# Kernel optimization log

Hardware: AMD Instinct MI355X
Metric: run time of the kernel (lower is better)

## Reference

```python
import jax, jax.numpy as jnp
import numpy as np


def setup_inputs() -> dict:
    key = jax.random.key(0)
    k1, k2, k3, k4 = jax.random.split(key, 4)
    B, S, IN, OUT = 4, 2048, 4096, 4096
    x = jax.random.normal(k1, (B, S, IN), dtype=jnp.float32)
    # 4-bit signed range [-8, 7], stored widened (torch uses int8)
    weight_quantized = jax.random.randint(k2, (OUT, IN), -8, 8, dtype=jnp.int32)
    # per-output-row scale, positive and small (abs-max / 7 style)
    weight_scale = jax.random.uniform(k3, (OUT,), dtype=jnp.float32) * 0.01 + 1e-4
    bias = jax.random.normal(k4, (OUT,), dtype=jnp.float32) * 0.01
    return {"x": x, "weight_quantized": weight_quantized,
            "weight_scale": weight_scale, "bias": bias}


def reference(x, weight_quantized, weight_scale, bias):
    # dequantize: [OUT, IN] int -> fp32 scaled per output row
    w = weight_quantized.astype(jnp.float32) * weight_scale[:, None]
    # F.linear: x @ w.T + bias  -> [B, S, OUT]
    out = jnp.einsum('bsi,oi->bso', x, w) + bias
    return out
```

## Files before the change

### kernel.cpp

```cpp
#include <hip/hip_runtime.h>
#include <hip/hip_bf16.h>

typedef __bf16 bf16x4 __attribute__((ext_vector_type(4)));
typedef __bf16 bf16x8 __attribute__((ext_vector_type(8)));
typedef float  floatx4 __attribute__((ext_vector_type(4)));

#define AS1 __attribute__((address_space(1)))
#define AS3 __attribute__((address_space(3)))

__global__ __launch_bounds__(256)
void cvt_both8(const float* __restrict__ xin, const int* __restrict__ win,
               __bf16* __restrict__ xout, __bf16* __restrict__ wout,
               int nx8, int nw8)
{
    const int stride = gridDim.x * 256;
    const int total  = nx8 + nw8;
    for (int i = blockIdx.x * 256 + threadIdx.x; i < total; i += stride) {
        if (i < nx8) {
            const float4* p = reinterpret_cast<const float4*>(xin) + (size_t)i * 2;
            float4 a = p[0], b = p[1];
            bf16x8 h;
            h[0] = (__bf16)a.x; h[1] = (__bf16)a.y; h[2] = (__bf16)a.z; h[3] = (__bf16)a.w;
            h[4] = (__bf16)b.x; h[5] = (__bf16)b.y; h[6] = (__bf16)b.z; h[7] = (__bf16)b.w;
            reinterpret_cast<bf16x8*>(xout)[i] = h;
        } else {
            int j = i - nx8;
            const int4* p = reinterpret_cast<const int4*>(win) + (size_t)j * 2;
            int4 a = p[0], b = p[1];
            bf16x8 h;
            h[0] = (__bf16)(float)a.x; h[1] = (__bf16)(float)a.y;
            h[2] = (__bf16)(float)a.z; h[3] = (__bf16)(float)a.w;
            h[4] = (__bf16)(float)b.x; h[5] = (__bf16)(float)b.y;
            h[6] = (__bf16)(float)b.z; h[7] = (__bf16)(float)b.w;
            reinterpret_cast<bf16x8*>(wout)[j] = h;
        }
    }
}

#define BM2 256
#define BN2 256
#define BK2 64

#define BARRIER() asm volatile("s_barrier" ::: "memory")

template<int P>
__device__ __forceinline__ void mfma_cluster(floatx4 (&acc)[8][4],
                                             const bf16x8 (&af)[2][2],
                                             const bf16x8 (&bfr)[4][2])
{
    __builtin_amdgcn_s_setprio(1);
#pragma unroll
    for (int h = 0; h < 2; ++h)
#pragma unroll
        for (int ii = 0; ii < 2; ++ii)
#pragma unroll
            for (int j = 0; j < 4; ++j)
                acc[2 * P + ii][j] = __builtin_amdgcn_mfma_f32_16x16x32_bf16(
                    af[ii][h], bfr[j][h], acc[2 * P + ii][j], 0, 0, 0);
    __builtin_amdgcn_s_setprio(0);
}

__device__ __forceinline__ void read_af(bf16x8 (&dst)[2][2], const __bf16* cA,
                                        int rowBase, int lm, int kq, int sw)
{
#pragma unroll
    for (int ii = 0; ii < 2; ++ii)
#pragma unroll
        for (int h = 0; h < 2; ++h)
            dst[ii][h] = *reinterpret_cast<const bf16x8*>(
                &cA[(rowBase + ii * 16 + lm) * BK2 + ((kq + h * 4) ^ sw) * 8]);
}

__device__ __forceinline__ void read_bf(bf16x8 (&dst)[4][2], const __bf16* cB,
                                        int wn, int lm, int kq, int sw)
{
#pragma unroll
    for (int j = 0; j < 4; ++j)
#pragma unroll
        for (int h = 0; h < 2; ++h)
            dst[j][h] = *reinterpret_cast<const bf16x8*>(
                &cB[(wn + j * 16 + lm) * BK2 + ((kq + h * 4) ^ sw) * 8]);
}

__global__ __launch_bounds__(512)
void gemm_bf16_bt_pipe(const __bf16* __restrict__ A, const __bf16* __restrict__ B,
                       const float* __restrict__ scale, const float* __restrict__ bias,
                       float* __restrict__ Out, int M, int N, int K)
{
    __shared__ __bf16 sA[2][BM2 * BK2];
    __shared__ __bf16 sB[2][BN2 * BK2];

    const int tid  = threadIdx.x;
    const int wave = tid >> 6;
    const int lane = tid & 63;
    const int row0 = blockIdx.y * BM2;
    const int col0 = blockIdx.x * BN2;

    const int sRow = lane >> 3;
    const int gBlk = (lane & 7) ^ sRow;
    const size_t aBase = (size_t)(row0 + wave * 8 + sRow) * K + gBlk * 8;
    const size_t bBase = (size_t)(col0 + wave * 8 + sRow) * K + gBlk * 8;
    const int ldsWOff = wave * 8 * BK2;

#define STAGE_A(buf, q, kt_) \
    __builtin_amdgcn_global_load_lds( \
        (const AS1 void*)(A + aBase + (size_t)(q) * 64 * K + (size_t)(kt_) * BK2), \
        (AS3 void*)&sA[(buf)][(q) * 64 * BK2 + ldsWOff], 16, 0, 0)
#define STAGE_B(buf, q, kt_) \
    __builtin_amdgcn_global_load_lds( \
        (const AS1 void*)(B + bBase + (size_t)(q) * 64 * K + (size_t)(kt_) * BK2), \
        (AS3 void*)&sB[(buf)][(q) * 64 * BK2 + ldsWOff], 16, 0, 0)

    const int wm = (wave >> 2) * 128;
    const int wn = (wave & 3) * 64;
    const int lm = lane & 15;
    const int kq = lane >> 4;
    const int sw = lm & 7;

    floatx4 acc[8][4];
#pragma unroll
    for (int i = 0; i < 8; ++i)
#pragma unroll
        for (int j = 0; j < 4; ++j)
            acc[i][j] = (floatx4)0.0f;

    bf16x8 bfr[4][2];
    bf16x8 afE[2][2];
    bf16x8 afO[2][2];
    const int nt = K / BK2;

    STAGE_A(0, 0, 0); STAGE_A(0, 2, 0);
    STAGE_B(0, 0, 0); STAGE_B(0, 1, 0); STAGE_B(0, 2, 0); STAGE_B(0, 3, 0);
    STAGE_A(0, 1, 0); STAGE_A(0, 3, 0);
    STAGE_B(1, 0, 1); STAGE_B(1, 1, 1); STAGE_B(1, 2, 1); STAGE_B(1, 3, 1);
    STAGE_A(1, 0, 1); STAGE_A(1, 2, 1);
    asm volatile("s_waitcnt vmcnt(8)" ::: "memory");
    BARRIER();
    read_bf(bfr, sB[0], wn, lm, kq, sw);
    read_af(afE, sA[0], wm, lm, kq, sw);

#define TILE(c, n1, n2)                                                        \
                                                                       \
    STAGE_A((c) ^ 1, 1, n1); STAGE_A((c) ^ 1, 3, n1);                          \
    mfma_cluster<0>(acc, afE, bfr);                                            \
    read_af(afO, sA[(c)], wm + 32, lm, kq, sw);                                \
    asm volatile("s_waitcnt vmcnt(8)" ::: "memory");                           \
    BARRIER();                                                                 \
                                                                       \
    STAGE_B((c), 0, n2); STAGE_B((c), 1, n2);                                  \
    STAGE_B((c), 2, n2); STAGE_B((c), 3, n2);                                  \
    mfma_cluster<1>(acc, afO, bfr);                                            \
    read_af(afE, sA[(c)], wm + 64, lm, kq, sw);                                \
    BARRIER();                                                                 \
                                                                       \
    STAGE_A((c), 0, n2); STAGE_A((c), 2, n2);                                  \
    mfma_cluster<2>(acc, afE, bfr);                                            \
    read_af(afO, sA[(c)], wm + 96, lm, kq, sw);                                \
    asm volatile("s_waitcnt vmcnt(8)" ::: "memory");                           \
    BARRIER();                                                                 \
                                                                       \
    mfma_cluster<3>(acc, afO, bfr);                                            \
    read_bf(bfr, sB[(c) ^ 1], wn, lm, kq, sw);                                 \
    read_af(afE, sA[(c) ^ 1], wm, lm, kq, sw);                                 \
    BARRIER();

    for (int it = 0; it < nt / 2; ++it) {
        const int kt = 2 * it;
        const int e1 = kt + 1;
        const int e2 = (kt + 2 < nt) ? kt + 2 : 0;
        const int o2 = (kt + 3 < nt) ? kt + 3 : 0;
        TILE(0, e1, e2)
        TILE(1, e2, o2)
    }
    asm volatile("s_waitcnt vmcnt(0)" ::: "memory");
#undef TILE
#undef STAGE_A
#undef STAGE_B

#pragma unroll
    for (int j = 0; j < 4; ++j) {
        int n = col0 + wn + j * 16 + lm;
        float sc = scale[n];
        float bi = bias[n];
#pragma unroll
        for (int i = 0; i < 8; ++i) {
#pragma unroll
            for (int r = 0; r < 4; ++r) {
                int m = row0 + wm + i * 16 + kq * 4 + r;
                Out[(size_t)m * N + n] = sc * acc[i][j][r] + bi;
            }
        }
    }
}

#define BM 128
#define BN 128
#define BK 64

__global__ __launch_bounds__(256)
void gemm_bf16_bt(const __bf16* __restrict__ A, const __bf16* __restrict__ B,
                  const float* __restrict__ scale, const float* __restrict__ bias,
                  float* __restrict__ Out, int M, int N, int K)
{
    __shared__ __bf16 sA[BM * BK];
    __shared__ __bf16 sB[BN * BK];

    const int tid  = threadIdx.x;
    const int row0 = blockIdx.y * BM;
    const int col0 = blockIdx.x * BN;
    const int wave = tid >> 6;
    const int lane = tid & 63;

    const int sRow = lane >> 3;
    const int gBlk = (lane & 7) ^ sRow;
    size_t aOff[4], bOff[4];
    const __bf16* ldsA[4];
    const __bf16* ldsB[4];
#pragma unroll
    for (int q = 0; q < 4; ++q) {
        int r = wave * 32 + q * 8 + sRow;
        aOff[q] = (size_t)(row0 + r) * K + gBlk * 8;
        bOff[q] = (size_t)(col0 + r) * K + gBlk * 8;
        ldsA[q] = &sA[(wave * 32 + q * 8) * BK];
        ldsB[q] = &sB[(wave * 32 + q * 8) * BK];
    }

    const int wm = (wave >> 1) * 64;
    const int wn = (wave & 1) * 64;
    const int lm = lane & 15;
    const int kq = lane >> 4;
    const int sw = lm & 7;

    floatx4 acc[4][4];
#pragma unroll
    for (int i = 0; i < 4; ++i)
#pragma unroll
        for (int j = 0; j < 4; ++j)
            acc[i][j] = (floatx4)0.0f;

    for (int k0 = 0; k0 < K; k0 += BK) {
#pragma unroll
        for (int q = 0; q < 4; ++q) {
            __builtin_amdgcn_global_load_lds((const AS1 void*)(A + aOff[q] + k0),
                                             (AS3 void*)ldsA[q], 16, 0, 0);
            __builtin_amdgcn_global_load_lds((const AS1 void*)(B + bOff[q] + k0),
                                             (AS3 void*)ldsB[q], 16, 0, 0);
        }
        __syncthreads();

#pragma unroll
        for (int h = 0; h < 2; ++h) {
            const int blkA = (kq + h * 4);
            bf16x8 af[4], bfr[4];
#pragma unroll
            for (int i = 0; i < 4; ++i) {
                int row = wm + i * 16 + lm;
                af[i] = *reinterpret_cast<const bf16x8*>(
                            &sA[row * BK + (blkA ^ sw) * 8]);
            }
#pragma unroll
            for (int j = 0; j < 4; ++j) {
                int row = wn + j * 16 + lm;
                bfr[j] = *reinterpret_cast<const bf16x8*>(
                            &sB[row * BK + (blkA ^ sw) * 8]);
            }
#pragma unroll
            for (int i = 0; i < 4; ++i)
#pragma unroll
                for (int j = 0; j < 4; ++j)
                    acc[i][j] = __builtin_amdgcn_mfma_f32_16x16x32_bf16(
                                    af[i], bfr[j], acc[i][j], 0, 0, 0);
        }
        __syncthreads();
    }

#pragma unroll
    for (int j = 0; j < 4; ++j) {
        int n = col0 + wn + j * 16 + lm;
        float sc = scale[n];
        float bi = bias[n];
#pragma unroll
        for (int i = 0; i < 4; ++i) {
#pragma unroll
            for (int r = 0; r < 4; ++r) {
                int m = row0 + wm + i * 16 + kq * 4 + r;
                Out[(size_t)m * N + n] = sc * acc[i][j][r] + bi;
            }
        }
    }
}

__global__ __launch_bounds__(256)
void fp4linear_gemm(const float* __restrict__ X, const int* __restrict__ W,
                    const float* __restrict__ scale, const float* __restrict__ bias,
                    float* __restrict__ Out, int M, int N, int K)
{
    __shared__ __bf16 sA[BM * 32];
    __shared__ __bf16 sB[BN * 32];

    const int tid  = threadIdx.x;
    const int row0 = blockIdx.y * BM;
    const int col0 = blockIdx.x * BN;
    const int wave = tid >> 6;
    const int lane = tid & 63;
    const int wm = (wave >> 1) * 64;
    const int wn = (wave & 1) * 64;
    const int lm = lane & 15;
    const int kq = lane >> 4;

    floatx4 acc[4][4];
#pragma unroll
    for (int i = 0; i < 4; ++i)
#pragma unroll
        for (int j = 0; j < 4; ++j)
            acc[i][j] = (floatx4)0.0f;

    for (int k0 = 0; k0 < K; k0 += 32) {
        float4 fa[4];
        int4   ib[4];
#pragma unroll
        for (int l = 0; l < 4; ++l) {
            int idx = tid + l * 256;
            int r = idx >> 3, c4 = idx & 7;
            fa[l] = *reinterpret_cast<const float4*>(
                        &X[(size_t)(row0 + r) * K + k0 + c4 * 4]);
        }
#pragma unroll
        for (int l = 0; l < 4; ++l) {
            int idx = tid + l * 256;
            int r = idx >> 3, c4 = idx & 7;
            ib[l] = *reinterpret_cast<const int4*>(
                        &W[(size_t)(col0 + r) * K + k0 + c4 * 4]);
        }
        __syncthreads();
#pragma unroll
        for (int l = 0; l < 4; ++l) {
            int idx = tid + l * 256;
            int r = idx >> 3, c4 = idx & 7;
            bf16x4 h;
            h[0] = (__bf16)fa[l].x; h[1] = (__bf16)fa[l].y;
            h[2] = (__bf16)fa[l].z; h[3] = (__bf16)fa[l].w;
            *reinterpret_cast<bf16x4*>(&sA[r * 32 + c4 * 4]) = h;
        }
#pragma unroll
        for (int l = 0; l < 4; ++l) {
            int idx = tid + l * 256;
            int r = idx >> 3, c4 = idx & 7;
            bf16x4 h;
            h[0] = (__bf16)(float)ib[l].x; h[1] = (__bf16)(float)ib[l].y;
            h[2] = (__bf16)(float)ib[l].z; h[3] = (__bf16)(float)ib[l].w;
            *reinterpret_cast<bf16x4*>(&sB[r * 32 + c4 * 4]) = h;
        }
        __syncthreads();

        bf16x8 af[4], bfr[4];
#pragma unroll
        for (int i = 0; i < 4; ++i)
            af[i] = *reinterpret_cast<const bf16x8*>(
                        &sA[(wm + i * 16 + lm) * 32 + kq * 8]);
#pragma unroll
        for (int j = 0; j < 4; ++j)
            bfr[j] = *reinterpret_cast<const bf16x8*>(
                        &sB[(wn + j * 16 + lm) * 32 + kq * 8]);
#pragma unroll
        for (int i = 0; i < 4; ++i)
#pragma unroll
            for (int j = 0; j < 4; ++j)
                acc[i][j] = __builtin_amdgcn_mfma_f32_16x16x32_bf16(
                                af[i], bfr[j], acc[i][j], 0, 0, 0);
    }

#pragma unroll
    for (int j = 0; j < 4; ++j) {
        int n = col0 + wn + j * 16 + lm;
        float sc = scale[n];
        float bi = bias[n];
#pragma unroll
        for (int i = 0; i < 4; ++i) {
#pragma unroll
            for (int r = 0; r < 4; ++r) {
                int m = row0 + wm + i * 16 + kq * 4 + r;
                Out[(size_t)m * N + n] = sc * acc[i][j][r] + bi;
            }
        }
    }
}

extern "C" void kernel_launch(void* const* d_in, const int* in_sizes, int n_in,
                              void* d_out, int out_size, void* d_ws, size_t ws_size,
                              hipStream_t stream) {
    const float* x     = (const float*)d_in[0];
    const int*   wq    = (const int*)d_in[1];
    const float* scale = (const float*)d_in[2];
    const float* bias  = (const float*)d_in[3];
    float* out = (float*)d_out;

    const int N = in_sizes[2];
    const int K = in_sizes[1] / N;
    const int M = in_sizes[0] / K;

    const size_t xElems = (size_t)M * K;
    const size_t wElems = (size_t)N * K;
    const size_t need   = (xElems + wElems) * sizeof(__bf16);

    const bool cvt_ok = (ws_size >= need) && (xElems % 8 == 0) && (wElems % 8 == 0);
    const int  nt     = K / BK2;

    if (cvt_ok) {
        __bf16* xb = (__bf16*)d_ws;
        __bf16* wb = xb + xElems;
        int nx8 = (int)(xElems / 8);
        int nw8 = (int)(wElems / 8);
        int total = nx8 + nw8;
        int cvtBlocks = (total + 255) / 256;
        if (cvtBlocks > 2048) cvtBlocks = 2048;
        hipLaunchKernelGGL(cvt_both8, dim3(cvtBlocks), dim3(256), 0, stream,
                           x, wq, xb, wb, nx8, nw8);
        if ((M % BM2 == 0) && (N % BN2 == 0) && (K % BK2 == 0) &&
            (nt % 2 == 0) && (nt >= 4)) {
            hipLaunchKernelGGL(gemm_bf16_bt_pipe, dim3(N / BN2, M / BM2), dim3(512),
                               0, stream, xb, wb, scale, bias, out, M, N, K);
        } else if ((M % BM == 0) && (N % BN == 0) && (K % BK == 0)) {
            hipLaunchKernelGGL(gemm_bf16_bt, dim3(N / BN, M / BM), dim3(256),
                               0, stream, xb, wb, scale, bias, out, M, N, K);
        } else {
            hipLaunchKernelGGL(fp4linear_gemm, dim3(N / BN, M / BM), dim3(256),
                               0, stream, x, wq, scale, bias, out, M, N, K);
        }
    } else {
        hipLaunchKernelGGL(fp4linear_gemm, dim3(N / BN, M / BM), dim3(256), 0, stream,
                           x, wq, scale, bias, out, M, N, K);
    }
}
```

Baseline: 507.0 us.

## Fuse conversion and GEMM into one cooperative persistent kernel with grid sync

Merges the fp32/int to bf16 conversion and the pipelined GEMM into a single cooperative kernel. The grid converts both operands, synchronizes across the whole grid, then loops persistently over 256x256 output tiles. This removes one kernel launch and the gap between kernels. The trade-offs are a grid-wide barrier, a grid capped at 256 blocks (so M=8192, N=4096 gives 512 tiles and two rounds per block), and slightly reordered LDS reads relative to the MFMA clusters. It also drops the 128x128 fallback GEMM path.

```diff
diff --git a/kernel.cpp b/kernel.cpp
--- a/kernel.cpp
+++ b/kernel.cpp
@@ -1,5 +1,8 @@
 #include <hip/hip_runtime.h>
 #include <hip/hip_bf16.h>
+#include <hip/hip_cooperative_groups.h>
+
+namespace cg = cooperative_groups;
 
 typedef __bf16 bf16x4 __attribute__((ext_vector_type(4)));
 typedef __bf16 bf16x8 __attribute__((ext_vector_type(8)));
@@ -7,6 +10,199 @@
 
 #define AS1 __attribute__((address_space(1)))
 #define AS3 __attribute__((address_space(3)))
+
+#define BM2 256
+#define BN2 256
+#define BK2 64
+
+#define BARRIER() asm volatile("s_barrier" ::: "memory")
+
+template<int P>
+__device__ __forceinline__ void mfma_cluster(floatx4 (&acc)[8][4],
+                                             const bf16x8 (&af)[2][2],
+                                             const bf16x8 (&bfr)[4][2])
+{
+    __builtin_amdgcn_s_setprio(1);
+#pragma unroll
+    for (int h = 0; h < 2; ++h)
+#pragma unroll
+        for (int ii = 0; ii < 2; ++ii)
+#pragma unroll
+            for (int j = 0; j < 4; ++j)
+                acc[2 * P + ii][j] = __builtin_amdgcn_mfma_f32_16x16x32_bf16(
+                    af[ii][h], bfr[j][h], acc[2 * P + ii][j], 0, 0, 0);
+    __builtin_amdgcn_s_setprio(0);
+}
+
+__device__ __forceinline__ void read_af(bf16x8 (&dst)[2][2], const __bf16* cA,
+                                        int rowBase, int lm, int kq, int sw)
+{
+#pragma unroll
+    for (int ii = 0; ii < 2; ++ii)
+#pragma unroll
+        for (int h = 0; h < 2; ++h)
+            dst[ii][h] = *reinterpret_cast<const bf16x8*>(
+                &cA[(rowBase + ii * 16 + lm) * BK2 + ((kq + h * 4) ^ sw) * 8]);
+}
+
+__device__ __forceinline__ void read_bf(bf16x8 (&dst)[4][2], const __bf16* cB,
+                                        int wn, int lm, int kq, int sw)
+{
+#pragma unroll
+    for (int j = 0; j < 4; ++j)
+#pragma unroll
+        for (int h = 0; h < 2; ++h)
+            dst[j][h] = *reinterpret_cast<const bf16x8*>(
+                &cB[(wn + j * 16 + lm) * BK2 + ((kq + h * 4) ^ sw) * 8]);
+}
+
+__device__ __forceinline__ void gemm_tile256(
+    __bf16* sAp, __bf16* sBp,
+    const __bf16* __restrict__ A, const __bf16* __restrict__ B,
+    const float* __restrict__ scale, const float* __restrict__ bias,
+    float* __restrict__ Out, int N, int K, int row0, int col0,
+    int wave, int lane)
+{
+    const int sRow = lane >> 3;
+    const int gBlk = (lane & 7) ^ sRow;
+    const size_t aBase = (size_t)(row0 + wave * 8 + sRow) * K + gBlk * 8;
+    const size_t bBase = (size_t)(col0 + wave * 8 + sRow) * K + gBlk * 8;
+    const int ldsWOff = wave * 8 * BK2;
+
+#define STAGE_A(buf, q, kt_) \
+    __builtin_amdgcn_global_load_lds( \
+        (const AS1 void*)(A + aBase + (size_t)(q) * 64 * K + (size_t)(kt_) * BK2), \
+        (AS3 void*)(sAp + (buf) * (BM2 * BK2) + (q) * 64 * BK2 + ldsWOff), 16, 0, 0)
+#define STAGE_B(buf, q, kt_) \
+    __builtin_amdgcn_global_load_lds( \
+        (const AS1 void*)(B + bBase + (size_t)(q) * 64 * K + (size_t)(kt_) * BK2), \
+        (AS3 void*)(sBp + (buf) * (BN2 * BK2) + (q) * 64 * BK2 + ldsWOff), 16, 0, 0)
+
+    const int wm = (wave >> 2) * 128;
+    const int wn = (wave & 3) * 64;
+    const int lm = lane & 15;
+    const int kq = lane >> 4;
+    const int sw = lm & 7;
+
+    floatx4 acc[8][4];
+#pragma unroll
+    for (int i = 0; i < 8; ++i)
+#pragma unroll
+        for (int j = 0; j < 4; ++j)
+            acc[i][j] = (floatx4)0.0f;
+
+    bf16x8 bfr[4][2];
+    bf16x8 afE[2][2];
+    bf16x8 afO[2][2];
+    const int nt = K / BK2;
+
+    STAGE_A(0, 0, 0); STAGE_A(0, 2, 0);
+    STAGE_B(0, 0, 0); STAGE_B(0, 1, 0); STAGE_B(0, 2, 0); STAGE_B(0, 3, 0);
+    STAGE_A(0, 1, 0); STAGE_A(0, 3, 0);
+    STAGE_B(1, 0, 1); STAGE_B(1, 1, 1); STAGE_B(1, 2, 1); STAGE_B(1, 3, 1);
+    STAGE_A(1, 0, 1); STAGE_A(1, 2, 1);
+    asm volatile("s_waitcnt vmcnt(8)" ::: "memory");
+    BARRIER();
+    read_bf(bfr, sBp, wn, lm, kq, sw);
+    read_af(afE, sAp, wm, lm, kq, sw);
+
+#define TILE(c, n1, n2)                                                        \
+                                                                       \
+    STAGE_A((c) ^ 1, 1, n1); STAGE_A((c) ^ 1, 3, n1);                          \
+    read_af(afO, sAp + (c) * (BM2 * BK2), wm + 32, lm, kq, sw);                \
+    mfma_cluster<0>(acc, afE, bfr);                                            \
+    asm volatile("s_waitcnt vmcnt(8)" ::: "memory");                           \
+    BARRIER();                                                                 \
+                                                                       \
+    STAGE_B((c), 0, n2); STAGE_B((c), 1, n2);                                  \
+    STAGE_B((c), 2, n2); STAGE_B((c), 3, n2);                                  \
+    read_af(afE, sAp + (c) * (BM2 * BK2), wm + 64, lm, kq, sw);                \
+    mfma_cluster<1>(acc, afO, bfr);                                            \
+    BARRIER();                                                                 \
+                                                                       \
+    STAGE_A((c), 0, n2); STAGE_A((c), 2, n2);                                  \
+    read_af(afO, sAp + (c) * (BM2 * BK2), wm + 96, lm, kq, sw);                \
+    mfma_cluster<2>(acc, afE, bfr);                                            \
+    asm volatile("s_waitcnt vmcnt(8)" ::: "memory");                           \
+    BARRIER();                                                                 \
+                                                                       \
+    read_af(afE, sAp + ((c) ^ 1) * (BM2 * BK2), wm, lm, kq, sw);               \
+    mfma_cluster<3>(acc, afO, bfr);                                            \
+    read_bf(bfr, sBp + ((c) ^ 1) * (BN2 * BK2), wn, lm, kq, sw);               \
+    BARRIER();
+
+    for (int it = 0; it < nt / 2; ++it) {
+        const int kt = 2 * it;
+        const int e1 = kt + 1;
+        const int e2 = (kt + 2 < nt) ? kt + 2 : 0;
+        const int o2 = (kt + 3 < nt) ? kt + 3 : 0;
+        TILE(0, e1, e2)
+        TILE(1, e2, o2)
+    }
+    asm volatile("s_waitcnt vmcnt(0)" ::: "memory");
+#undef TILE
+#undef STAGE_A
+#undef STAGE_B
+
+#pragma unroll
+    for (int j = 0; j < 4; ++j) {
+        int n = col0 + wn + j * 16 + lm;
+        float sc = scale[n];
+        float bi = bias[n];
+#pragma unroll
+        for (int i = 0; i < 8; ++i) {
+#pragma unroll
+            for (int r = 0; r < 4; ++r) {
+                int m = row0 + wm + i * 16 + kq * 4 + r;
+                Out[(size_t)m * N + n] = sc * acc[i][j][r] + bi;
+            }
+        }
+    }
+}
+
+__global__ __launch_bounds__(512)
+void fused_coop(const float* __restrict__ xin, const int* __restrict__ win,
+                const float* __restrict__ scale, const float* __restrict__ bias,
+                float* __restrict__ out, __bf16* __restrict__ xb,
+                __bf16* __restrict__ wb, int M, int N, int K, int nx8, int nw8)
+{
+    {
+        const int stride = gridDim.x * 512;
+        const int total  = nx8 + nw8;
+        for (int i = blockIdx.x * 512 + threadIdx.x; i < total; i += stride) {
+            if (i < nx8) {
+                const float4* p = reinterpret_cast<const float4*>(xin) + (size_t)i * 2;
+                float4 a = p[0], b = p[1];
+                bf16x8 h;
+                h[0] = (__bf16)a.x; h[1] = (__bf16)a.y; h[2] = (__bf16)a.z; h[3] = (__bf16)a.w;
+                h[4] = (__bf16)b.x; h[5] = (__bf16)b.y; h[6] = (__bf16)b.z; h[7] = (__bf16)b.w;
+                reinterpret_cast<bf16x8*>(xb)[i] = h;
+            } else {
+                int j = i - nx8;
+                const int4* p = reinterpret_cast<const int4*>(win) + (size_t)j * 2;
+                int4 a = p[0], b = p[1];
+                bf16x8 h;
+                h[0] = (__bf16)(float)a.x; h[1] = (__bf16)(float)a.y;
+                h[2] = (__bf16)(float)a.z; h[3] = (__bf16)(float)a.w;
+                h[4] = (__bf16)(float)b.x; h[5] = (__bf16)(float)b.y;
+                h[6] = (__bf16)(float)b.z; h[7] = (__bf16)(float)b.w;
+                reinterpret_cast<bf16x8*>(wb)[j] = h;
+            }
+        }
+    }
+    cg::this_grid().sync();
+
+    __shared__ __bf16 sA[2 * BM2 * BK2];
+    __shared__ __bf16 sB[2 * BN2 * BK2];
+    const int wave = threadIdx.x >> 6;
+    const int lane = threadIdx.x & 63;
+    const int nbx = N / BN2;
+    const int nTiles = (M / BM2) * nbx;
+    for (int t = blockIdx.x; t < nTiles; t += gridDim.x) {
+        gemm_tile256(sA, sB, xb, wb, scale, bias, out, N, K,
+                     (t / nbx) * BM2, (t % nbx) * BN2, wave, lane);
+    }
+}
 
 __global__ __launch_bounds__(256)
 void cvt_both8(const float* __restrict__ xin, const int* __restrict__ win,
@@ -37,258 +233,20 @@
     }
 }
 
-#define BM2 256
-#define BN2 256
-#define BK2 64
-
-#define BARRIER() asm volatile("s_barrier" ::: "memory")
-
-template<int P>
-__device__ __forceinline__ void mfma_cluster(floatx4 (&acc)[8][4],
-                                             const bf16x8 (&af)[2][2],
-                                             const bf16x8 (&bfr)[4][2])
-{
-    __builtin_amdgcn_s_setprio(1);
-#pragma unroll
-    for (int h = 0; h < 2; ++h)
-#pragma unroll
-        for (int ii = 0; ii < 2; ++ii)
-#pragma unroll
-            for (int j = 0; j < 4; ++j)
-                acc[2 * P + ii][j] = __builtin_amdgcn_mfma_f32_16x16x32_bf16(
-                    af[ii][h], bfr[j][h], acc[2 * P + ii][j], 0, 0, 0);
-    __builtin_amdgcn_s_setprio(0);
-}
-
-__device__ __forceinline__ void read_af(bf16x8 (&dst)[2][2], const __bf16* cA,
-                                        int rowBase, int lm, int kq, int sw)
-{
-#pragma unroll
-    for (int ii = 0; ii < 2; ++ii)
-#pragma unroll
-        for (int h = 0; h < 2; ++h)
-            dst[ii][h] = *reinterpret_cast<const bf16x8*>(
-                &cA[(rowBase + ii * 16 + lm) * BK2 + ((kq + h * 4) ^ sw) * 8]);
-}
-
-__device__ __forceinline__ void read_bf(bf16x8 (&dst)[4][2], const __bf16* cB,
-                                        int wn, int lm, int kq, int sw)
-{
-#pragma unroll
-    for (int j = 0; j < 4; ++j)
-#pragma unroll
-        for (int h = 0; h < 2; ++h)
-            dst[j][h] = *reinterpret_cast<const bf16x8*>(
-                &cB[(wn + j * 16 + lm) * BK2 + ((kq + h * 4) ^ sw) * 8]);
-}
-
 __global__ __launch_bounds__(512)
 void gemm_bf16_bt_pipe(const __bf16* __restrict__ A, const __bf16* __restrict__ B,
                        const float* __restrict__ scale, const float* __restrict__ bias,
                        float* __restrict__ Out, int M, int N, int K)
 {
-    __shared__ __bf16 sA[2][BM2 * BK2];
-    __shared__ __bf16 sB[2][BN2 * BK2];
-
-    const int tid  = threadIdx.x;
-    const int wave = tid >> 6;
-    const int lane = tid & 63;
-    const int row0 = blockIdx.y * BM2;
-    const int col0 = blockIdx.x * BN2;
-
-    const int sRow = lane >> 3;
-    const int gBlk = (lane & 7) ^ sRow;
-    const size_t aBase = (size_t)(row0 + wave * 8 + sRow) * K + gBlk * 8;
-    const size_t bBase = (size_t)(col0 + wave * 8 + sRow) * K + gBlk * 8;
-    const int ldsWOff = wave * 8 * BK2;
-
-#define STAGE_A(buf, q, kt_) \
-    __builtin_amdgcn_global_load_lds( \
-        (const AS1 void*)(A + aBase + (size_t)(q) * 64 * K + (size_t)(kt_) * BK2), \
-        (AS3 void*)&sA[(buf)][(q) * 64 * BK2 + ldsWOff], 16, 0, 0)
-#define STAGE_B(buf, q, kt_) \
-    __builtin_amdgcn_global_load_lds( \
-        (const AS1 void*)(B + bBase + (size_t)(q) * 64 * K + (size_t)(kt_) * BK2), \
-        (AS3 void*)&sB[(buf)][(q) * 64 * BK2 + ldsWOff], 16, 0, 0)
-
-    const int wm = (wave >> 2) * 128;
-    const int wn = (wave & 3) * 64;
-    const int lm = lane & 15;
-    const int kq = lane >> 4;
-    const int sw = lm & 7;
-
-    floatx4 acc[8][4];
-#pragma unroll
-    for (int i = 0; i < 8; ++i)
-#pragma unroll
-        for (int j = 0; j < 4; ++j)
-            acc[i][j] = (floatx4)0.0f;
-
-    bf16x8 bfr[4][2];
-    bf16x8 afE[2][2];
-    bf16x8 afO[2][2];
-    const int nt = K / BK2;
-
-    STAGE_A(0, 0, 0); STAGE_A(0, 2, 0);
-    STAGE_B(0, 0, 0); STAGE_B(0, 1, 0); STAGE_B(0, 2, 0); STAGE_B(0, 3, 0);
-    STAGE_A(0, 1, 0); STAGE_A(0, 3, 0);
-    STAGE_B(1, 0, 1); STAGE_B(1, 1, 1); STAGE_B(1, 2, 1); STAGE_B(1, 3, 1);
-    STAGE_A(1, 0, 1); STAGE_A(1, 2, 1);
-    asm volatile("s_waitcnt vmcnt(8)" ::: "memory");
-    BARRIER();
-    read_bf(bfr, sB[0], wn, lm, kq, sw);
-    read_af(afE, sA[0], wm, lm, kq, sw);
-
-#define TILE(c, n1, n2)                                                        \
-                                                                       \
-    STAGE_A((c) ^ 1, 1, n1); STAGE_A((c) ^ 1, 3, n1);                          \
-    mfma_cluster<0>(acc, afE, bfr);                                            \
-    read_af(afO, sA[(c)], wm + 32, lm, kq, sw);                                \
-    asm volatile("s_waitcnt vmcnt(8)" ::: "memory");                           \
-    BARRIER();                                                                 \
-                                                                       \
-    STAGE_B((c), 0, n2); STAGE_B((c), 1, n2);                                  \
-    STAGE_B((c), 2, n2); STAGE_B((c), 3, n2);                                  \
-    mfma_cluster<1>(acc, afO, bfr);                                            \
-    read_af(afE, sA[(c)], wm + 64, lm, kq, sw);                                \
-    BARRIER();                                                                 \
-                                                                       \
-    STAGE_A((c), 0, n2); STAGE_A((c), 2, n2);                                  \
-    mfma_cluster<2>(acc, afE, bfr);                                            \
-    read_af(afO, sA[(c)], wm + 96, lm, kq, sw);                                \
-    asm volatile("s_waitcnt vmcnt(8)" ::: "memory");                           \
-    BARRIER();                                                                 \
-                                                                       \
-    mfma_cluster<3>(acc, afO, bfr);                                            \
-    read_bf(bfr, sB[(c) ^ 1], wn, lm, kq, sw);                                 \
-    read_af(afE, sA[(c) ^ 1], wm, lm, kq, sw);                                 \
-    BARRIER();
-
-    for (int it = 0; it < nt / 2; ++it) {
-        const int kt = 2 * it;
-        const int e1 = kt + 1;
-        const int e2 = (kt + 2 < nt) ? kt + 2 : 0;
-        const int o2 = (kt + 3 < nt) ? kt + 3 : 0;
-        TILE(0, e1, e2)
-        TILE(1, e2, o2)
-    }
-    asm volatile("s_waitcnt vmcnt(0)" ::: "memory");
-#undef TILE
-#undef STAGE_A
-#undef STAGE_B
-
-#pragma unroll
-    for (int j = 0; j < 4; ++j) {
-        int n = col0 + wn + j * 16 + lm;
-        float sc = scale[n];
-        float bi = bias[n];
-#pragma unroll
-        for (int i = 0; i < 8; ++i) {
-#pragma unroll
-            for (int r = 0; r < 4; ++r) {
-                int m = row0 + wm + i * 16 + kq * 4 + r;
-                Out[(size_t)m * N + n] = sc * acc[i][j][r] + bi;
-            }
-        }
-    }
+    __shared__ __bf16 sA[2 * BM2 * BK2];
+    __shared__ __bf16 sB[2 * BN2 * BK2];
+    gemm_tile256(sA, sB, A, B, scale, bias, Out, N, K,
+                 blockIdx.y * BM2, blockIdx.x * BN2,
+                 threadIdx.x >> 6, threadIdx.x & 63);
 }
 
 #define BM 128
 #define BN 128
-#define BK 64
-
-__global__ __launch_bounds__(256)
-void gemm_bf16_bt(const __bf16* __restrict__ A, const __bf16* __restrict__ B,
-                  const float* __restrict__ scale, const float* __restrict__ bias,
-                  float* __restrict__ Out, int M, int N, int K)
-{
-    __shared__ __bf16 sA[BM * BK];
-    __shared__ __bf16 sB[BN * BK];
-
-    const int tid  = threadIdx.x;
-    const int row0 = blockIdx.y * BM;
-    const int col0 = blockIdx.x * BN;
-    const int wave = tid >> 6;
-    const int lane = tid & 63;
-
-    const int sRow = lane >> 3;
-    const int gBlk = (lane & 7) ^ sRow;
-    size_t aOff[4], bOff[4];
-    const __bf16* ldsA[4];
-    const __bf16* ldsB[4];
-#pragma unroll
-    for (int q = 0; q < 4; ++q) {
-        int r = wave * 32 + q * 8 + sRow;
-        aOff[q] = (size_t)(row0 + r) * K + gBlk * 8;
-        bOff[q] = (size_t)(col0 + r) * K + gBlk * 8;
-        ldsA[q] = &sA[(wave * 32 + q * 8) * BK];
-        ldsB[q] = &sB[(wave * 32 + q * 8) * BK];
-    }
-
-    const int wm = (wave >> 1) * 64;
-    const int wn = (wave & 1) * 64;
-    const int lm = lane & 15;
-    const int kq = lane >> 4;
-    const int sw = lm & 7;
-
-    floatx4 acc[4][4];
-#pragma unroll
-    for (int i = 0; i < 4; ++i)
-#pragma unroll
-        for (int j = 0; j < 4; ++j)
-            acc[i][j] = (floatx4)0.0f;
-
-    for (int k0 = 0; k0 < K; k0 += BK) {
-#pragma unroll
-        for (int q = 0; q < 4; ++q) {
-            __builtin_amdgcn_global_load_lds((const AS1 void*)(A + aOff[q] + k0),
-                                             (AS3 void*)ldsA[q], 16, 0, 0);
-            __builtin_amdgcn_global_load_lds((const AS1 void*)(B + bOff[q] + k0),
-                                             (AS3 void*)ldsB[q], 16, 0, 0);
-        }
-        __syncthreads();
-
-#pragma unroll
-        for (int h = 0; h < 2; ++h) {
-            const int blkA = (kq + h * 4);
-            bf16x8 af[4], bfr[4];
-#pragma unroll
-            for (int i = 0; i < 4; ++i) {
-                int row = wm + i * 16 + lm;
-                af[i] = *reinterpret_cast<const bf16x8*>(
-                            &sA[row * BK + (blkA ^ sw) * 8]);
-            }
-#pragma unroll
-            for (int j = 0; j < 4; ++j) {
-                int row = wn + j * 16 + lm;
-                bfr[j] = *reinterpret_cast<const bf16x8*>(
-                            &sB[row * BK + (blkA ^ sw) * 8]);
-            }
-#pragma unroll
-            for (int i = 0; i < 4; ++i)
-#pragma unroll
-                for (int j = 0; j < 4; ++j)
-                    acc[i][j] = __builtin_amdgcn_mfma_f32_16x16x32_bf16(
-                                    af[i], bfr[j], acc[i][j], 0, 0, 0);
-        }
-        __syncthreads();
-    }
-
-#pragma unroll
-    for (int j = 0; j < 4; ++j) {
-        int n = col0 + wn + j * 16 + lm;
-        float sc = scale[n];
-        float bi = bias[n];
-#pragma unroll
-        for (int i = 0; i < 4; ++i) {
-#pragma unroll
-            for (int r = 0; r < 4; ++r) {
-                int m = row0 + wm + i * 16 + kq * 4 + r;
-                Out[(size_t)m * N + n] = sc * acc[i][j][r] + bi;
-            }
-        }
-    }
-}
 
 __global__ __launch_bounds__(256)
 void fp4linear_gemm(const float* __restrict__ X, const int* __restrict__ W,
@@ -405,30 +363,36 @@
 
     const bool cvt_ok = (ws_size >= need) && (xElems % 8 == 0) && (wElems % 8 == 0);
     const int  nt     = K / BK2;
-
-    if (cvt_ok) {
+    const bool gemm_ok = (M % BM2 == 0) && (N % BN2 == 0) && (K % BK2 == 0) &&
+                         (nt % 2 == 0) && (nt >= 4);
+
+    if (cvt_ok && gemm_ok) {
         __bf16* xb = (__bf16*)d_ws;
         __bf16* wb = xb + xElems;
         int nx8 = (int)(xElems / 8);
         int nw8 = (int)(wElems / 8);
+        int nTiles = (M / BM2) * (N / BN2);
+        int coopBlocks = nTiles < 256 ? nTiles : 256;
+
+        void* args[] = { (void*)&x, (void*)&wq, (void*)&scale, (void*)&bias,
+                         (void*)&out, (void*)&xb, (void*)&wb,
+                         (void*)&M, (void*)&N, (void*)&K,
+                         (void*)&nx8, (void*)&nw8 };
+        hipError_t e = hipLaunchCooperativeKernel((void*)fused_coop,
+                                                  dim3(coopBlocks), dim3(512),
+                                                  args, 0, stream);
+        if (e == hipSuccess) return;
+
         int total = nx8 + nw8;
         int cvtBlocks = (total + 255) / 256;
         if (cvtBlocks > 2048) cvtBlocks = 2048;
         hipLaunchKernelGGL(cvt_both8, dim3(cvtBlocks), dim3(256), 0, stream,
                            x, wq, xb, wb, nx8, nw8);
-        if ((M % BM2 == 0) && (N % BN2 == 0) && (K % BK2 == 0) &&
-            (nt % 2 == 0) && (nt >= 4)) {
-            hipLaunchKernelGGL(gemm_bf16_bt_pipe, dim3(N / BN2, M / BM2), dim3(512),
-                               0, stream, xb, wb, scale, bias, out, M, N, K);
-        } else if ((M % BM == 0) && (N % BN == 0) && (K % BK == 0)) {
-            hipLaunchKernelGGL(gemm_bf16_bt, dim3(N / BN, M / BM), dim3(256),
-                               0, stream, xb, wb, scale, bias, out, M, N, K);
-        } else {
-            hipLaunchKernelGGL(fp4linear_gemm, dim3(N / BN, M / BM), dim3(256),
-                               0, stream, x, wq, scale, bias, out, M, N, K);
-        }
-    } else {
-        hipLaunchKernelGGL(fp4linear_gemm, dim3(N / BN, M / BM), dim3(256), 0, stream,
-                           x, wq, scale, bias, out, M, N, K);
-    }
-}
+        hipLaunchKernelGGL(gemm_bf16_bt_pipe, dim3(N / BN2, M / BM2), dim3(512),
+                           0, stream, xb, wb, scale, bias, out, M, N, K);
+        return;
+    }
+
+    hipLaunchKernelGGL(fp4linear_gemm, dim3(N / BN, M / BM), dim3(256), 0, stream,
+                       x, wq, scale, bias, out, M, N, K);
+}
```

Result: slower. 602.4 us (+18.8%).
